# Kernel optimization log

Hardware: AMD Instinct MI355X
Metric: run time of the kernel (lower is better)

The kernel has to match this reference:

```python
import jax, jax.numpy as jnp
import numpy as np

BN_EPS = 1e-5


def setup_inputs() -> dict:
    key = jax.random.key(0)
    ks = jax.random.split(key, 8)
    N, C, H, W = 16, 64, 56, 56
    Ch = C // 2
    x = jax.random.normal(ks[0], (N, C, H, W), dtype=jnp.float32)
    # 1x1 convs represented as [out, in] matrices
    w1 = jax.random.normal(ks[1], (Ch, C), dtype=jnp.float32) / np.sqrt(C)
    b1 = jnp.zeros((Ch,), dtype=jnp.float32)
    w2 = jax.random.normal(ks[2], (Ch, C), dtype=jnp.float32) / np.sqrt(C)
    b2 = jnp.zeros((Ch,), dtype=jnp.float32)
    w3 = jax.random.normal(ks[3], (C, C), dtype=jnp.float32) / np.sqrt(C)
    b3 = jnp.zeros((C,), dtype=jnp.float32)
    gamma = jnp.ones((C,), dtype=jnp.float32)
    beta = jnp.zeros((C,), dtype=jnp.float32)
    return {"x": x, "w1": w1, "b1": b1, "w2": w2, "b2": b2,
            "w3": w3, "b3": b3, "gamma": gamma, "beta": beta}


def _conv1x1(x, w, b):
    # x: [N,C,H,W], w: [O,C] -> [N,O,H,W]
    return jnp.einsum('nchw,oc->nohw', x, w) + b[None, :, None, None]


def reference(x, w1, b1, w2, b2, w3, b3, gamma, beta):
    N, C, H, W = x.shape
    S = H * W
    theta = _conv1x1(x, w1, b1)            # [N, C/2, H, W]
    phi = _conv1x1(x, w2, b2)              # [N, C/2, H, W]
    g = x                                  # [N, C, H, W]
    th = theta.reshape(N, -1, S)           # [N, C/2, S]
    ph = phi.reshape(N, -1, S)             # [N, C/2, S]
    gf = g.reshape(N, C, S)                # [N, C, S]
    scale = 1.0 / jnp.sqrt(jnp.float32(th.shape[1]))
    attn = jnp.einsum('nis,nit->nst', th, ph) * scale   # [N, S, S]
    attn = jax.nn.softmax(attn, axis=-1)
    f = jnp.einsum('nst,nit->nis', attn, gf).reshape(N, C, H, W)
    f = _conv1x1(f, w3, b3)
    # BatchNorm2d, training mode (batch statistics, biased variance)
    mean = jnp.mean(f, axis=(0, 2, 3), keepdims=True)
    var = jnp.mean((f - mean) ** 2, axis=(0, 2, 3), keepdims=True)
    f = (f - mean) / jnp.sqrt(var + BN_EPS)
    f = f * gamma[None, :, None, None] + beta[None, :, None, None]
    return x + f
```

## Files before the change

kernel.cpp:

```cpp
#include <hip/hip_runtime.h>
#include <hip/hip_bf16.h>

constexpr int N_ = 16, C_ = 64, CH_ = 32;
constexpr int S_ = 3136;
constexpr int SB = 64;
constexpr int NB = S_ / SB;
constexpr float SCALE = 0.17677669529663687f;
constexpr float LOG2E = 1.4426950408889634f;
constexpr float SCALE2 = SCALE * LOG2E;
constexpr float FIXM2 = 16.0f * LOG2E;

using f32x4 = __attribute__((ext_vector_type(4))) float;
using f32x16 = __attribute__((ext_vector_type(16))) float;
using bf16x8 = __attribute__((ext_vector_type(8))) short;
using u32x2 = __attribute__((ext_vector_type(2))) unsigned;
using u32x4 = __attribute__((ext_vector_type(4))) unsigned;

__device__ __forceinline__ unsigned cvtpk(float lo, float hi) {
  unsigned r;
  asm("v_cvt_pk_bf16_f32 %0, %1, %2" : "=v"(r) : "v"(lo), "v"(hi));
  return r;
}
__device__ __forceinline__ float exp2a(float x) {
  float r;
  asm("v_exp_f32 %0, %1" : "=v"(r) : "v"(x));
  return r;
}
__device__ __forceinline__ unsigned short f2bf(float f) {
  unsigned int u = __builtin_bit_cast(unsigned int, f);
  u += 0x7fffu + ((u >> 16) & 1u);
  return (unsigned short)(u >> 16);
}

__global__ __launch_bounds__(256)
void prep_kernel(const float* __restrict__ x,
                 const float* __restrict__ w1, const float* __restrict__ b1,
                 const float* __restrict__ w2, const float* __restrict__ b2,
                 unsigned short* __restrict__ thetaT,
                 unsigned short* __restrict__ phiT,
                 unsigned short* __restrict__ xbf) {
  __shared__ float xl[64][68];
  __shared__ __align__(16) unsigned short thL[64][40];
  __shared__ __align__(16) unsigned short phL[64][40];
  const int b = blockIdx.x;
  const int n = b / NB;
  const int s0 = (b % NB) * SB;
  const int tid = threadIdx.x;
  const int sl = tid & 63;
  const int grp = tid >> 6;

#pragma unroll
  for (int cc = 0; cc < 4; ++cc) {
    int c = cc * 16 + grp * 4 + (sl >> 4);
    int s4 = (sl & 15) * 4;
    size_t gidx = (size_t)(n * C_ + c) * S_ + s0 + s4;
    f32x4 v = *(const f32x4*)(x + gidx);
    *(f32x4*)&xl[c][s4] = v;
    u32x2 pb;
    pb.x = cvtpk(v[0], v[1]);
    pb.y = cvtpk(v[2], v[3]);
    *(u32x2*)(xbf + gidx) = pb;
  }
  __syncthreads();

  float acc1[8], acc2[8];
  const int i0u = __builtin_amdgcn_readfirstlane(grp * 8);
  const float* w1b = w1 + i0u * C_;
  const float* w2b = w2 + i0u * C_;
#pragma unroll
  for (int ii = 0; ii < 8; ++ii) {
    acc1[ii] = b1[i0u + ii];
    acc2[ii] = b2[i0u + ii];
  }
#pragma unroll 1
  for (int cc = 0; cc < 4; ++cc) {
    float xv[16];
#pragma unroll
    for (int k = 0; k < 16; ++k) xv[k] = xl[cc * 16 + k][sl];
#pragma unroll
    for (int ii = 0; ii < 8; ++ii) {
#pragma unroll
      for (int k = 0; k < 16; ++k) {
        acc1[ii] = fmaf(w1b[ii * C_ + cc * 16 + k], xv[k], acc1[ii]);
        acc2[ii] = fmaf(w2b[ii * C_ + cc * 16 + k], xv[k], acc2[ii]);
      }
    }
  }
  {
    u32x4 t4, p4;
    t4.x = cvtpk(acc1[0] * SCALE2, acc1[1] * SCALE2);
    t4.y = cvtpk(acc1[2] * SCALE2, acc1[3] * SCALE2);
    t4.z = cvtpk(acc1[4] * SCALE2, acc1[5] * SCALE2);
    t4.w = cvtpk(acc1[6] * SCALE2, acc1[7] * SCALE2);
    p4.x = cvtpk(acc2[0], acc2[1]);
    p4.y = cvtpk(acc2[2], acc2[3]);
    p4.z = cvtpk(acc2[4], acc2[5]);
    p4.w = cvtpk(acc2[6], acc2[7]);
    *(u32x4*)&thL[sl][grp * 8] = t4;
    *(u32x4*)&phL[sl][grp * 8] = p4;
  }
  __syncthreads();
  {
    int row = tid >> 2, ch = (tid & 3) * 8;
    size_t o = ((size_t)(n * S_) + s0 + row) * CH_ + ch;
    *(bf16x8*)(thetaT + o) = *(const bf16x8*)&thL[row][ch];
    *(bf16x8*)(phiT + o)   = *(const bf16x8*)&phL[row][ch];
  }
}

__global__ __launch_bounds__(256)
void attn_kernel(const unsigned short* __restrict__ thetaT,
                 const unsigned short* __restrict__ phiT,
                 const unsigned short* __restrict__ xbf,
                 const float* __restrict__ w3, const float* __restrict__ b3,
                 unsigned short* __restrict__ yb, float* __restrict__ partials) {
  __shared__ __align__(16) unsigned short ldsK[2][64 * 40];
  __shared__ __align__(16) unsigned short ldsV[2][64 * 72];
  __shared__ float redS[2][128];
  const int b = (blockIdx.x & 7) * 98 + (blockIdx.x >> 3);
  const int n = b / NB;
  const int q0 = (b % NB) * SB;
  const int tid = threadIdx.x;
  const int lane = tid & 63;
  const int w = tid >> 6;
  const int qw = w & 1;
  const int th = w >> 1;
  const int cl = lane & 31;
  const int h = lane >> 5;

  const unsigned short* thQ =
      thetaT + ((size_t)(n * S_) + q0 + qw * 32 + cl) * CH_;
  const bf16x8 qfA = *(const bf16x8*)(thQ + h * 8);
  const bf16x8 qfB = *(const bf16x8*)(thQ + 16 + h * 8);

  f32x16 oacc[2];
#pragma unroll
  for (int cb = 0; cb < 2; ++cb)
#pragma unroll
    for (int r = 0; r < 16; ++r) oacc[cb][r] = 0.f;
  float lsum = 0.f;
  f32x16 cinit;
#pragma unroll
  for (int r = 0; r < 16; ++r) cinit[r] = -FIXM2;

  const unsigned short* phiB = phiT + (size_t)n * S_ * CH_;
  const unsigned short* vB = xbf + (size_t)n * C_ * S_;

  const int krow = tid >> 2, kch = (tid & 3) * 8;
  const int vc = tid >> 3, vch = (tid & 7) * 8;

  bf16x8 kst, vst0, vst1;
  kst = *(const bf16x8*)(phiB + (size_t)krow * CH_ + kch);
  vst0 = *(const bf16x8*)(vB + (size_t)vc * S_ + vch);
  vst1 = *(const bf16x8*)(vB + (size_t)(vc + 32) * S_ + vch);
  *(bf16x8*)(ldsK[0] + krow * 40 + kch) = kst;
  *(bf16x8*)(ldsV[0] + vc * 72 + vch) = vst0;
  *(bf16x8*)(ldsV[0] + (vc + 32) * 72 + vch) = vst1;
  __syncthreads();

  int cur = 0;
#pragma unroll 1
  for (int t0 = 0; t0 < S_; t0 += 64) {
    const bool pre = (t0 + 64 < S_);
    if (pre) {
      kst = *(const bf16x8*)(phiB + (size_t)(t0 + 64 + krow) * CH_ + kch);
      vst0 = *(const bf16x8*)(vB + (size_t)vc * S_ + t0 + 64 + vch);
      vst1 = *(const bf16x8*)(vB + (size_t)(vc + 32) * S_ + t0 + 64 + vch);
    }

    const unsigned short* Kc = ldsK[cur];
    const unsigned short* Vc = ldsV[cur];

    const unsigned short* kr = Kc + (th * 32 + cl) * 40 + h * 8;
    bf16x8 kfA = *(const bf16x8*)(kr);
    bf16x8 kfB = *(const bf16x8*)(kr + 16);
    __builtin_amdgcn_s_setprio(1);
    f32x16 st = __builtin_amdgcn_mfma_f32_32x32x16_bf16(kfA, qfA, cinit, 0, 0, 0);
    st = __builtin_amdgcn_mfma_f32_32x32x16_bf16(kfB, qfB, st, 0, 0, 0);
    __builtin_amdgcn_s_setprio(0);

    float p[16];
#pragma unroll
    for (int r = 0; r < 16; ++r) {
      p[r] = exp2a(st[r]);
      lsum += p[r];
    }
    unsigned pkw[8];
#pragma unroll
    for (int i = 0; i < 8; ++i) pkw[i] = cvtpk(p[2 * i], p[2 * i + 1]);

    __builtin_amdgcn_s_setprio(1);
#pragma unroll
    for (int tb = 0; tb < 2; ++tb) {
      bf16x8 pf = __builtin_bit_cast(bf16x8,
          (u32x4){pkw[tb * 4 + 0], pkw[tb * 4 + 1], pkw[tb * 4 + 2], pkw[tb * 4 + 3]});
#pragma unroll
      for (int cb = 0; cb < 2; ++cb) {
        const unsigned short* vr =
            Vc + (cb * 32 + cl) * 72 + th * 32 + tb * 16 + 4 * h;
        u32x2 v0 = *(const u32x2*)(vr);
        u32x2 v1 = *(const u32x2*)(vr + 8);
        bf16x8 vf = __builtin_bit_cast(bf16x8, (u32x4){v0.x, v0.y, v1.x, v1.y});
        oacc[cb] = __builtin_amdgcn_mfma_f32_32x32x16_bf16(vf, pf, oacc[cb], 0, 0, 0);
      }
    }
    __builtin_amdgcn_s_setprio(0);

    if (pre) {
      *(bf16x8*)(ldsK[cur ^ 1] + krow * 40 + kch) = kst;
      *(bf16x8*)(ldsV[cur ^ 1] + vc * 72 + vch) = vst0;
      *(bf16x8*)(ldsV[cur ^ 1] + (vc + 32) * 72 + vch) = vst1;
    }
    __syncthreads();
    cur ^= 1;
  }

  float* mrg = (float*)&ldsV[0][0];
  if (th == 1) {
    float* pm = mrg + ((size_t)(qw * 64 + lane)) * 36;
#pragma unroll
    for (int cb = 0; cb < 2; ++cb)
#pragma unroll
      for (int i = 0; i < 4; ++i) {
        f32x4 v = {oacc[cb][4 * i], oacc[cb][4 * i + 1],
                   oacc[cb][4 * i + 2], oacc[cb][4 * i + 3]};
        *(f32x4*)(pm + cb * 16 + 4 * i) = v;
      }
    pm[32] = lsum;
  }
  __syncthreads();
  if (th == 0) {
    float* pm = mrg + ((size_t)(qw * 64 + lane)) * 36;
#pragma unroll
    for (int cb = 0; cb < 2; ++cb)
#pragma unroll
      for (int i = 0; i < 4; ++i) {
        f32x4 v = *(const f32x4*)(pm + cb * 16 + 4 * i);
        oacc[cb][4 * i] += v[0];
        oacc[cb][4 * i + 1] += v[1];
        oacc[cb][4 * i + 2] += v[2];
        oacc[cb][4 * i + 3] += v[3];
      }
    lsum += pm[32];

    float lt = lsum;
    lt += __shfl_xor(lt, 32);
    const float inv = 1.0f / lt;

    unsigned ff[4][4];
#pragma unroll
    for (int kb = 0; kb < 4; ++kb) {
      const int blk = kb >> 1, rb = (kb & 1) * 8;
#pragma unroll
      for (int i = 0; i < 4; ++i)
        ff[kb][i] = cvtpk(oacc[blk][rb + 2 * i] * inv,
                          oacc[blk][rb + 2 * i + 1] * inv);
    }

    const int q = q0 + qw * 32 + cl;
#pragma unroll
    for (int ch32 = 0; ch32 < 2; ++ch32) {
      const float* wr = w3 + (ch32 * 32 + cl) * C_;
      f32x16 acc;
      {
        f32x4 b0 = *(const f32x4*)(b3 + ch32 * 32 + 4 * h);
        f32x4 b1v = *(const f32x4*)(b3 + ch32 * 32 + 8 + 4 * h);
        f32x4 b2v = *(const f32x4*)(b3 + ch32 * 32 + 16 + 4 * h);
        f32x4 b3v = *(const f32x4*)(b3 + ch32 * 32 + 24 + 4 * h);
#pragma unroll
        for (int i = 0; i < 4; ++i) {
          acc[i] = b0[i];
          acc[4 + i] = b1v[i];
          acc[8 + i] = b2v[i];
          acc[12 + i] = b3v[i];
        }
      }
#pragma unroll
      for (int kb = 0; kb < 4; ++kb) {
        f32x4 a0 = *(const f32x4*)(wr + kb * 16 + 4 * h);
        f32x4 a1 = *(const f32x4*)(wr + kb * 16 + 8 + 4 * h);
        u32x4 wf;
        wf.x = cvtpk(a0[0], a0[1]);
        wf.y = cvtpk(a0[2], a0[3]);
        wf.z = cvtpk(a1[0], a1[1]);
        wf.w = cvtpk(a1[2], a1[3]);
        bf16x8 fb = __builtin_bit_cast(bf16x8,
            (u32x4){ff[kb][0], ff[kb][1], ff[kb][2], ff[kb][3]});
        acc = __builtin_amdgcn_mfma_f32_32x32x16_bf16(
            __builtin_bit_cast(bf16x8, wf), fb, acc, 0, 0, 0);
      }
#pragma unroll
      for (int r = 0; r < 16; ++r) {
        const int co = ch32 * 32 + (r & 3) + 8 * (r >> 2) + 4 * h;
        float yv = acc[r];
        yb[(size_t)(n * C_ + co) * S_ + q] = f2bf(yv);
        float s1 = yv, s2 = yv * yv;
#pragma unroll
        for (int off = 1; off < 32; off <<= 1) {
          s1 += __shfl_xor(s1, off);
          s2 += __shfl_xor(s2, off);
        }
        if (cl == 0) {
          redS[qw][co] = s1;
          redS[qw][64 + co] = s2;
        }
      }
    }
  }
  __syncthreads();
  if (tid < 128)
    partials[(size_t)b * 128 + tid] = redS[0][tid] + redS[1][tid];
}

__global__ __launch_bounds__(256)
void stats_kernel(const float* __restrict__ partials, float* __restrict__ stats) {
  __shared__ float red[4];
  const int c = blockIdx.x;
  const int tid = threadIdx.x;
  float s = 0.f;
  for (int r = tid; r < N_ * NB; r += 256) s += partials[(size_t)r * 128 + c];
#pragma unroll
  for (int off = 1; off < 64; off <<= 1) s += __shfl_xor(s, off);
  if ((tid & 63) == 0) red[tid >> 6] = s;
  __syncthreads();
  if (tid == 0) stats[c] = red[0] + red[1] + red[2] + red[3];
}

__global__ __launch_bounds__(256)
void bn_kernel(const float* __restrict__ x, const unsigned short* __restrict__ yb,
               const float* __restrict__ stats,
               const float* __restrict__ gamma, const float* __restrict__ beta,
               float* __restrict__ out) {
  const int idx = blockIdx.x * 256 + threadIdx.x;
  const size_t base = (size_t)idx * 8;
  const int c = (int)((base / S_) & 63);
  constexpr float invcnt = 1.0f / (N_ * S_);
  float mean = stats[c] * invcnt;
  float var = stats[64 + c] * invcnt - mean * mean;
  float a = gamma[c] * rsqrtf(var + 1e-5f);
  float bb = beta[c] - mean * a;
  u32x4 yv = *(const u32x4*)(yb + base);
#pragma unroll
  for (int hh = 0; hh < 2; ++hh) {
    f32x4 xv = *(const f32x4*)(x + base + hh * 4);
    f32x4 o;
#pragma unroll
    for (int r = 0; r < 2; ++r) {
      unsigned packed = (hh * 2 + r == 0) ? yv.x : (hh * 2 + r == 1) ? yv.y
                        : (hh * 2 + r == 2) ? yv.z : yv.w;
      float ylo = __builtin_bit_cast(float, packed << 16);
      float yhi = __builtin_bit_cast(float, packed & 0xffff0000u);
      o[r * 2 + 0] = fmaf(ylo, a, xv[r * 2 + 0] + bb);
      o[r * 2 + 1] = fmaf(yhi, a, xv[r * 2 + 1] + bb);
    }
    *(f32x4*)(out + base + hh * 4) = o;
  }
}

extern "C" void kernel_launch(void* const* d_in, const int* in_sizes, int n_in,
                              void* d_out, int out_size, void* d_ws, size_t ws_size,
                              hipStream_t stream) {
  const float* x = (const float*)d_in[0];
  const float* w1 = (const float*)d_in[1];
  const float* b1 = (const float*)d_in[2];
  const float* w2 = (const float*)d_in[3];
  const float* b2 = (const float*)d_in[4];
  const float* w3 = (const float*)d_in[5];
  const float* b3 = (const float*)d_in[6];
  const float* gamma = (const float*)d_in[7];
  const float* beta = (const float*)d_in[8];

  char* ws = (char*)d_ws;
  unsigned short* thetaT = (unsigned short*)(ws + 0);
  unsigned short* phiT   = (unsigned short*)(ws + 3211264);
  unsigned short* xbf    = (unsigned short*)(ws + 6422528);
  unsigned short* yb     = (unsigned short*)(ws + 12845056);
  float* stats           = (float*)(ws + 19267584);
  float* partials        = (float*)(ws + 19268096);
  if (ws_size < 19669504) return;

  prep_kernel<<<N_ * NB, 256, 0, stream>>>(x, w1, b1, w2, b2, thetaT, phiT, xbf);
  attn_kernel<<<N_ * NB, 256, 0, stream>>>(thetaT, phiT, xbf, w3, b3, yb, partials);
  stats_kernel<<<128, 256, 0, stream>>>(partials, stats);
  bn_kernel<<<(out_size / 8) / 256, 256, 0, stream>>>(x, yb, stats, gamma, beta, (float*)d_out);
}
```

Measured before the change: 102.6 us.

## Stream V tiles via direct global-to-LDS loads with XOR swizzle; read bf16 residual

The attention kernel now loads V tiles with global_load_lds straight into an unpadded, XOR-swizzled LDS layout. This drops the register staging and the padding, and the MFMA operand reads use precomputed swizzled offsets. The merge buffer is also swizzled and the lsum values move to a separate array. The BN kernel reads the residual x from the bf16 copy instead of fp32, halving that read traffic but adding bf16 rounding error to the residual term of the output.

```diff
diff --git a/kernel.cpp b/kernel.cpp
--- a/kernel.cpp
+++ b/kernel.cpp
@@ -115,8 +115,9 @@
                  const float* __restrict__ w3, const float* __restrict__ b3,
                  unsigned short* __restrict__ yb, float* __restrict__ partials) {
   __shared__ __align__(16) unsigned short ldsK[2][64 * 40];
-  __shared__ __align__(16) unsigned short ldsV[2][64 * 72];
+  __shared__ __align__(16) unsigned short ldsV[2][64 * 64];
   __shared__ float redS[2][128];
+  __shared__ float lsumX[128];
   const int b = (blockIdx.x & 7) * 98 + (blockIdx.x >> 3);
   const int n = b / NB;
   const int q0 = (b % NB) * SB;
@@ -147,15 +148,32 @@
   const unsigned short* vB = xbf + (size_t)n * C_ * S_;
 
   const int krow = tid >> 2, kch = (tid & 3) * 8;
-  const int vc = tid >> 3, vch = (tid & 7) * 8;
-
-  bf16x8 kst, vst0, vst1;
-  kst = *(const bf16x8*)(phiB + (size_t)krow * CH_ + kch);
-  vst0 = *(const bf16x8*)(vB + (size_t)vc * S_ + vch);
-  vst1 = *(const bf16x8*)(vB + (size_t)(vc + 32) * S_ + vch);
-  *(bf16x8*)(ldsK[0] + krow * 40 + kch) = kst;
-  *(bf16x8*)(ldsV[0] + vc * 72 + vch) = vst0;
-  *(bf16x8*)(ldsV[0] + (vc + 32) * 72 + vch) = vst1;
+  const int vcj = w * 8 + (lane >> 3);
+  const unsigned short* vsrc0 = vB + (size_t)vcj * S_ + (((lane & 7) ^ (lane >> 3)) * 8);
+  const unsigned short* vsrc1 = vsrc0 + (size_t)32 * S_;
+  const int vdst = w * 512;
+
+  const int swu = (cl & 7) << 3;
+  int vOffA[2][2], vOffB[2][2];
+#pragma unroll
+  for (int tb = 0; tb < 2; ++tb)
+#pragma unroll
+    for (int cb = 0; cb < 2; ++cb) {
+      const int c = cb * 32 + cl;
+      const int tau = th * 32 + tb * 16 + 4 * h;
+      vOffA[tb][cb] = c * 64 + (tau ^ swu);
+      vOffB[tb][cb] = c * 64 + ((tau + 8) ^ swu);
+    }
+
+  bf16x8 kst;
+  {
+    kst = *(const bf16x8*)(phiB + (size_t)krow * CH_ + kch);
+    __builtin_amdgcn_global_load_lds((const unsigned int*)(vsrc0),
+                                     (unsigned int*)(ldsV[0] + vdst), 16, 0, 0);
+    __builtin_amdgcn_global_load_lds((const unsigned int*)(vsrc1),
+                                     (unsigned int*)(ldsV[0] + 2048 + vdst), 16, 0, 0);
+    *(bf16x8*)(ldsK[0] + krow * 40 + kch) = kst;
+  }
   __syncthreads();
 
   int cur = 0;
@@ -164,8 +182,10 @@
     const bool pre = (t0 + 64 < S_);
     if (pre) {
       kst = *(const bf16x8*)(phiB + (size_t)(t0 + 64 + krow) * CH_ + kch);
-      vst0 = *(const bf16x8*)(vB + (size_t)vc * S_ + t0 + 64 + vch);
-      vst1 = *(const bf16x8*)(vB + (size_t)(vc + 32) * S_ + t0 + 64 + vch);
+      __builtin_amdgcn_global_load_lds((const unsigned int*)(vsrc0 + t0 + 64),
+                                       (unsigned int*)(ldsV[cur ^ 1] + vdst), 16, 0, 0);
+      __builtin_amdgcn_global_load_lds((const unsigned int*)(vsrc1 + t0 + 64),
+                                       (unsigned int*)(ldsV[cur ^ 1] + 2048 + vdst), 16, 0, 0);
     }
 
     const unsigned short* Kc = ldsK[cur];
@@ -196,10 +216,8 @@
           (u32x4){pkw[tb * 4 + 0], pkw[tb * 4 + 1], pkw[tb * 4 + 2], pkw[tb * 4 + 3]});
 #pragma unroll
       for (int cb = 0; cb < 2; ++cb) {
-        const unsigned short* vr =
-            Vc + (cb * 32 + cl) * 72 + th * 32 + tb * 16 + 4 * h;
-        u32x2 v0 = *(const u32x2*)(vr);
-        u32x2 v1 = *(const u32x2*)(vr + 8);
+        u32x2 v0 = *(const u32x2*)(Vc + vOffA[tb][cb]);
+        u32x2 v1 = *(const u32x2*)(Vc + vOffB[tb][cb]);
         bf16x8 vf = __builtin_bit_cast(bf16x8, (u32x4){v0.x, v0.y, v1.x, v1.y});
         oacc[cb] = __builtin_amdgcn_mfma_f32_32x32x16_bf16(vf, pf, oacc[cb], 0, 0, 0);
       }
@@ -208,40 +226,39 @@
 
     if (pre) {
       *(bf16x8*)(ldsK[cur ^ 1] + krow * 40 + kch) = kst;
-      *(bf16x8*)(ldsV[cur ^ 1] + vc * 72 + vch) = vst0;
-      *(bf16x8*)(ldsV[cur ^ 1] + (vc + 32) * 72 + vch) = vst1;
     }
     __syncthreads();
     cur ^= 1;
   }
 
   float* mrg = (float*)&ldsV[0][0];
+  const int msw = (lane & 7) << 2;
   if (th == 1) {
-    float* pm = mrg + ((size_t)(qw * 64 + lane)) * 36;
+    float* pm = mrg + (qw * 64 + lane) * 32;
 #pragma unroll
     for (int cb = 0; cb < 2; ++cb)
 #pragma unroll
       for (int i = 0; i < 4; ++i) {
         f32x4 v = {oacc[cb][4 * i], oacc[cb][4 * i + 1],
                    oacc[cb][4 * i + 2], oacc[cb][4 * i + 3]};
-        *(f32x4*)(pm + cb * 16 + 4 * i) = v;
-      }
-    pm[32] = lsum;
+        *(f32x4*)(pm + ((cb * 16 + i * 4) ^ msw)) = v;
+      }
+    lsumX[qw * 64 + lane] = lsum;
   }
   __syncthreads();
   if (th == 0) {
-    float* pm = mrg + ((size_t)(qw * 64 + lane)) * 36;
+    float* pm = mrg + (qw * 64 + lane) * 32;
 #pragma unroll
     for (int cb = 0; cb < 2; ++cb)
 #pragma unroll
       for (int i = 0; i < 4; ++i) {
-        f32x4 v = *(const f32x4*)(pm + cb * 16 + 4 * i);
+        f32x4 v = *(const f32x4*)(pm + ((cb * 16 + i * 4) ^ msw));
         oacc[cb][4 * i] += v[0];
         oacc[cb][4 * i + 1] += v[1];
         oacc[cb][4 * i + 2] += v[2];
         oacc[cb][4 * i + 3] += v[3];
       }
-    lsum += pm[32];
+    lsum += lsumX[qw * 64 + lane];
 
     float lt = lsum;
     lt += __shfl_xor(lt, 32);
@@ -327,7 +344,8 @@
 }
 
 __global__ __launch_bounds__(256)
-void bn_kernel(const float* __restrict__ x, const unsigned short* __restrict__ yb,
+void bn_kernel(const unsigned short* __restrict__ xbf,
+               const unsigned short* __restrict__ yb,
                const float* __restrict__ stats,
                const float* __restrict__ gamma, const float* __restrict__ beta,
                float* __restrict__ out) {
@@ -340,18 +358,21 @@
   float a = gamma[c] * rsqrtf(var + 1e-5f);
   float bb = beta[c] - mean * a;
   u32x4 yv = *(const u32x4*)(yb + base);
+  u32x4 xv = *(const u32x4*)(xbf + base);
 #pragma unroll
   for (int hh = 0; hh < 2; ++hh) {
-    f32x4 xv = *(const f32x4*)(x + base + hh * 4);
     f32x4 o;
 #pragma unroll
     for (int r = 0; r < 2; ++r) {
-      unsigned packed = (hh * 2 + r == 0) ? yv.x : (hh * 2 + r == 1) ? yv.y
-                        : (hh * 2 + r == 2) ? yv.z : yv.w;
-      float ylo = __builtin_bit_cast(float, packed << 16);
-      float yhi = __builtin_bit_cast(float, packed & 0xffff0000u);
-      o[r * 2 + 0] = fmaf(ylo, a, xv[r * 2 + 0] + bb);
-      o[r * 2 + 1] = fmaf(yhi, a, xv[r * 2 + 1] + bb);
+      const int wsel = hh * 2 + r;
+      unsigned py = (wsel == 0) ? yv.x : (wsel == 1) ? yv.y : (wsel == 2) ? yv.z : yv.w;
+      unsigned px = (wsel == 0) ? xv.x : (wsel == 1) ? xv.y : (wsel == 2) ? xv.z : xv.w;
+      float ylo = __builtin_bit_cast(float, py << 16);
+      float yhi = __builtin_bit_cast(float, py & 0xffff0000u);
+      float xlo = __builtin_bit_cast(float, px << 16);
+      float xhi = __builtin_bit_cast(float, px & 0xffff0000u);
+      o[r * 2 + 0] = fmaf(ylo, a, xlo + bb);
+      o[r * 2 + 1] = fmaf(yhi, a, xhi + bb);
     }
     *(f32x4*)(out + base + hh * 4) = o;
   }
@@ -382,5 +403,5 @@
   prep_kernel<<<N_ * NB, 256, 0, stream>>>(x, w1, b1, w2, b2, thetaT, phiT, xbf);
   attn_kernel<<<N_ * NB, 256, 0, stream>>>(thetaT, phiT, xbf, w3, b3, yb, partials);
   stats_kernel<<<128, 256, 0, stream>>>(partials, stats);
-  bn_kernel<<<(out_size / 8) / 256, 256, 0, stream>>>(x, yb, stats, gamma, beta, (float*)d_out);
-}
+  bn_kernel<<<(out_size / 8) / 256, 256, 0, stream>>>(xbf, yb, stats, gamma, beta, (float*)d_out);
+}
```

After: 108.8 us. 6.0% more time.
